# Performance work log

Measured on AMD Instinct MI355X. Metric: run time of the kernel, lower is better.

The kernel has to match this reference:

```python
import jax, jax.numpy as jnp
import numpy as np

N_EMBD = 2048
N_HEAD = 32
N_KV_HEAD = 8
HEAD_DIM = N_EMBD // N_HEAD  # 64
N_REP = N_HEAD // N_KV_HEAD  # 4
WINDOW = 1024
ROPE_BASE = 10000.0


def setup_inputs() -> dict:
    key = jax.random.key(0)
    ks = jax.random.split(key, 4)
    B, T = 2, 4096
    x = jax.random.normal(ks[0], (B, T, N_EMBD), dtype=jnp.float32)
    s = 0.02
    Wq = jax.random.normal(ks[1], (N_EMBD, N_HEAD * HEAD_DIM), dtype=jnp.float32) * s
    Wkv = jax.random.normal(ks[2], (N_EMBD, 2 * N_KV_HEAD * HEAD_DIM), dtype=jnp.float32) * s
    Wo = jax.random.normal(ks[3], (N_EMBD, N_EMBD), dtype=jnp.float32) * s
    return {"x": x, "Wq": Wq, "Wkv": Wkv, "Wo": Wo}


def _rotate_half(x):
    x1, x2 = jnp.split(x, 2, axis=-1)
    return jnp.concatenate([-x2, x1], axis=-1)


def _rope_cos_sin(T, dtype):
    inv_freq = 1.0 / (ROPE_BASE ** (jnp.arange(0, HEAD_DIM, 2, dtype=jnp.float32) / HEAD_DIM))
    t = jnp.arange(T, dtype=jnp.float32)
    freqs = jnp.einsum("i,j->ij", t, inv_freq)  # [T, HEAD_DIM/2]
    emb = jnp.concatenate([freqs, freqs], axis=-1)  # [T, HEAD_DIM]
    return jnp.cos(emb).astype(dtype)[None, None], jnp.sin(emb).astype(dtype)[None, None]


def reference(x, Wq, Wkv, Wo):
    B, T, _ = x.shape
    q = (x @ Wq).reshape(B, T, N_HEAD, HEAD_DIM).transpose(0, 2, 1, 3)  # [B,H,T,D]
    kv = (x @ Wkv).reshape(B, T, 2, N_KV_HEAD, HEAD_DIM)
    k = kv[:, :, 0].transpose(0, 2, 1, 3)  # [B,KV,T,D]
    v = kv[:, :, 1].transpose(0, 2, 1, 3)

    cos, sin = _rope_cos_sin(T, x.dtype)
    q = q * cos + _rotate_half(q) * sin
    k = k * cos + _rotate_half(k) * sin

    # repeat kv heads for GQA: [B,KV,T,D] -> [B,H,T,D]
    k = jnp.repeat(k, N_REP, axis=1)
    v = jnp.repeat(v, N_REP, axis=1)

    scale = 1.0 / jnp.sqrt(jnp.asarray(HEAD_DIM, dtype=x.dtype))
    scores = jnp.einsum("bhqd,bhkd->bhqk", q, k) * scale  # [B,H,T,T]

    # causal + sliding window mask: attend iff q - window < kpos <= qpos
    qpos = jnp.arange(T)[:, None]
    kpos = jnp.arange(T)[None, :]
    allowed = (kpos <= qpos) & (kpos > qpos - WINDOW)
    scores = jnp.where(allowed[None, None], scores, jnp.asarray(-jnp.inf, dtype=scores.dtype))

    attn = jax.nn.softmax(scores, axis=-1)
    out = jnp.einsum("bhqk,bhkd->bhqd", attn, v)  # [B,H,T,D]
    out = out.transpose(0, 2, 1, 3).reshape(B, T, N_EMBD)
    return out @ Wo
```

## Files before the change

### kernel.cpp

```cpp
#include <hip/hip_runtime.h>
#include <cstddef>

typedef unsigned short ushort_t;
typedef unsigned int uint32;

typedef __bf16   bf16x8 __attribute__((ext_vector_type(8)));
typedef __bf16   bf16x2 __attribute__((ext_vector_type(2)));
typedef __bf16   bf16x4 __attribute__((ext_vector_type(4)));
typedef float    f32x16 __attribute__((ext_vector_type(16)));
typedef float    f32x4  __attribute__((ext_vector_type(4)));
typedef ushort_t u16x8  __attribute__((ext_vector_type(8)));
typedef ushort_t u16x4  __attribute__((ext_vector_type(4)));
typedef uint32   u32x4  __attribute__((ext_vector_type(4)));
typedef uint32   u32x2  __attribute__((ext_vector_type(2)));

__device__ __forceinline__ ushort_t f2b(float f) {
  uint32 u = __builtin_bit_cast(uint32, f);
  u += 0x7fff + ((u >> 16) & 1);
  return (ushort_t)(u >> 16);
}

__device__ __forceinline__ f32x16 mfma32(bf16x8 a, bf16x8 b, f32x16 c) {
  return __builtin_amdgcn_mfma_f32_32x32x16_bf16(a, b, c, 0, 0, 0);
}

__device__ __forceinline__ void gload_lds16(const void* g, void* l) {
  __builtin_amdgcn_global_load_lds((const __attribute__((address_space(1))) void*)g,
                                   (__attribute__((address_space(3))) void*)l, 16, 0, 0);
}

__launch_bounds__(256)
__global__ void k_prep(const float* __restrict__ x, ushort_t* __restrict__ x_c, int nCvt,
                       const float* __restrict__ Wq, ushort_t* __restrict__ WqT,
                       const float* __restrict__ Wkv, ushort_t* __restrict__ WkvT,
                       const float* __restrict__ Wo, ushort_t* __restrict__ WoT,
                       float* __restrict__ cosT, float* __restrict__ sinT) {
  __shared__ __align__(16) ushort_t tile[64][72];
  const int tid = threadIdx.x;
  int bid = blockIdx.x;
  if (bid < 512) {
    int idx = bid * 256 + tid;
    int t = idx >> 5, j = idx & 31;
    float invf = __expf(-(float)j * (9.210340371976184f / 32.0f));
    float ang = (float)t * invf;
    cosT[idx] = cosf(ang);
    sinT[idx] = sinf(ang);
    return;
  }
  bid -= 512;
  if (bid < nCvt) {
    size_t i = ((size_t)bid * 256 + tid) * 8;
    f32x4 a = *(const f32x4*)(x + i);
    f32x4 b = *(const f32x4*)(x + i + 4);
    u16x8 v = {f2b(a[0]), f2b(a[1]), f2b(a[2]), f2b(a[3]),
               f2b(b[0]), f2b(b[1]), f2b(b[2]), f2b(b[3])};
    *(u16x8*)(x_c + i) = v;
    return;
  }
  bid -= nCvt;
  const float* W;
  ushort_t* Wt;
  int N;
  if (bid < 1024)      { W = Wq;  Wt = WqT;  N = 2048; }
  else if (bid < 1536) { W = Wkv; Wt = WkvT; N = 1024; bid -= 1024; }
  else                 { W = Wo;  Wt = WoT;  N = 2048; bid -= 1536; }
  const int K = 2048;
  int nbx = N >> 6;
  int bx = bid % nbx, by = bid / nbx;
  int r0 = by << 6, c0 = bx << 6;
#pragma unroll
  for (int p = 0; p < 2; p++) {
    int id = p * 256 + tid;
    int r = id >> 3, cs = id & 7;
    const float* src = W + (size_t)(r0 + r) * N + c0 + cs * 8;
    f32x4 a = *(const f32x4*)(src);
    f32x4 b = *(const f32x4*)(src + 4);
    u16x8 v = {f2b(a[0]), f2b(a[1]), f2b(a[2]), f2b(a[3]),
               f2b(b[0]), f2b(b[1]), f2b(b[2]), f2b(b[3])};
    *(u16x8*)&tile[r][cs * 8] = v;
  }
  __syncthreads();
#pragma unroll
  for (int p = 0; p < 2; p++) {
    int id = p * 256 + tid;
    int oc = id >> 3, ocs = id & 7;
    u16x8 v;
#pragma unroll
    for (int j = 0; j < 8; j++) v[j] = tile[ocs * 8 + j][oc];
    *(u16x8*)(Wt + (size_t)(c0 + oc) * K + r0 + ocs * 8) = v;
  }
}

__launch_bounds__(256)
__global__ void k_gemm_qkv(const ushort_t* __restrict__ A,
                           const ushort_t* __restrict__ BtQ,
                           const ushort_t* __restrict__ BtKV, int M,
                           ushort_t* __restrict__ qout, ushort_t* __restrict__ kout,
                           ushort_t* __restrict__ vout,
                           const float* __restrict__ cosT,
                           const float* __restrict__ sinT) {
  __shared__ __align__(16) ushort_t lds[2][2][128 * 32];
  const int tid = threadIdx.x;
  const int wave = tid >> 6, lane = tid & 63;
  const int l31 = lane & 31, hf = lane >> 5;
  const int K = 2048;
  const int bid = (int)blockIdx.x;
  const int blk = (bid & 7) * (int)(gridDim.x >> 3) + (bid >> 3);
  const int nQ = (M >> 7) << 4;
  const bool isQ = blk < nQ;
  int sub = isQ ? blk : blk - nQ;
  const int nTn = isQ ? 16 : 8;
  const ushort_t* Bt = isQ ? BtQ : BtKV;
  const int st = sub >> 4, si = sub & 15;
  const int nStc = nTn >> 2;
  const int stm = st / nStc, stn = st % nStc;
  const int bm = stm * 4 + (si >> 2), bn = stn * 4 + (si & 3);
  const int row0 = bm << 7, col0 = bn << 7;

  f32x16 acc[2][2] = {};

  auto stage = [&](int buf, int k0) {
#pragma unroll
    for (int side = 0; side < 2; side++) {
      const ushort_t* src = side ? Bt : A;
      int r0g = side ? col0 : row0;
#pragma unroll
      for (int i = 0; i < 2; i++) {
        int rl = wave * 32 + i * 16 + (lane >> 2);
        int cs = lane & 3;
        const ushort_t* gp = src + (size_t)(r0g + rl) * K + k0 + cs * 8;
        ushort_t* lp = &lds[buf][side][(wave * 32 + i * 16) * 32];
        gload_lds16(gp, lp);
      }
    }
  };

  stage(0, 0);
  __syncthreads();

  const int wm = wave >> 1, wn = wave & 1;
  const int nk = K >> 5;
  for (int kt = 0; kt < nk; kt++) {
    const int buf = kt & 1;
    if (kt + 1 < nk) stage(buf ^ 1, (kt + 1) << 5);
    const ushort_t* la = &lds[buf][0][0];
    const ushort_t* lb = &lds[buf][1][0];
#pragma unroll
    for (int ks = 0; ks < 2; ks++) {
      const int kc = ks * 2 + hf;
      bf16x8 af[2], bg[2];
#pragma unroll
      for (int mi = 0; mi < 2; mi++) {
        int r = wm * 64 + mi * 32 + l31;
        af[mi] = *(const bf16x8*)(la + r * 32 + kc * 8);
      }
#pragma unroll
      for (int ni = 0; ni < 2; ni++) {
        int r = wn * 64 + ni * 32 + l31;
        bg[ni] = *(const bf16x8*)(lb + r * 32 + kc * 8);
      }
#pragma unroll
      for (int mi = 0; mi < 2; mi++)
#pragma unroll
        for (int ni = 0; ni < 2; ni++)
          acc[mi][ni] = mfma32(af[mi], bg[ni], acc[mi][ni]);
    }
    __syncthreads();
  }

  if (isQ) {
    int cg = col0 + wn * 64 + l31;
#pragma unroll
    for (int mi = 0; mi < 2; mi++)
#pragma unroll
      for (int r = 0; r < 16; r++) {
        int rg = row0 + wm * 64 + mi * 32 + (r & 3) + 8 * (r >> 2) + 4 * hf;
        int t = rg & 4095;
        float c = cosT[t * 32 + l31];
        float s = sinT[t * 32 + l31];
        float lo = acc[mi][0][r], hi = acc[mi][1][r];
        qout[(size_t)rg * 2048 + cg]      = f2b(lo * c - hi * s);
        qout[(size_t)rg * 2048 + cg + 32] = f2b(hi * c + lo * s);
      }
  } else {
    int cb = col0 + wn * 64;
    if (cb < 512) {
      int g = cb >> 6;
#pragma unroll
      for (int mi = 0; mi < 2; mi++)
#pragma unroll
        for (int r = 0; r < 16; r++) {
          int rg = row0 + wm * 64 + mi * 32 + (r & 3) + 8 * (r >> 2) + 4 * hf;
          int t = rg & 4095, b = rg >> 12;
          float c = cosT[t * 32 + l31];
          float s = sinT[t * 32 + l31];
          float lo = acc[mi][0][r], hi = acc[mi][1][r];
          size_t base = ((size_t)(b * 8 + g) * 4096 + t) * 64;
          kout[base + l31]      = f2b(lo * c - hi * s);
          kout[base + l31 + 32] = f2b(hi * c + lo * s);
        }
    } else {
#pragma unroll
      for (int mi = 0; mi < 2; mi++)
#pragma unroll
        for (int ni = 0; ni < 2; ni++) {
          int vd = cb + ni * 32 + l31 - 512;
          int g = vd >> 6, d = vd & 63;
#pragma unroll
          for (int g2 = 0; g2 < 4; g2++) {
            int rg = row0 + wm * 64 + mi * 32 + 8 * g2 + 4 * hf;
            int b = rg >> 12, tl = rg & 4095;
            u16x4 pk = {f2b(acc[mi][ni][g2 * 4 + 0]), f2b(acc[mi][ni][g2 * 4 + 1]),
                        f2b(acc[mi][ni][g2 * 4 + 2]), f2b(acc[mi][ni][g2 * 4 + 3])};
            size_t base = (((size_t)(b * 8 + g) * 128 + (tl >> 5)) * 64 + d) * 32;
            int vtl = 16 * (g2 >> 1) + 8 * hf + 4 * (g2 & 1);
            *(u16x4*)(vout + base + vtl) = pk;
          }
        }
    }
  }
}

__launch_bounds__(256)
__global__ void k_gemm_o(const ushort_t* __restrict__ A, const ushort_t* __restrict__ Bt,
                         int M, float* __restrict__ outf) {
  __shared__ __align__(16) ushort_t lds[2][2][128 * 32];
  const int tid = threadIdx.x;
  const int wave = tid >> 6, lane = tid & 63;
  const int l31 = lane & 31, hf = lane >> 5;
  const int K = 2048, N = 2048, nTn = 16;
  const int bid = (int)blockIdx.x;
  const int blk = (bid & 7) * (int)(gridDim.x >> 3) + (bid >> 3);
  const int st = blk >> 4, si = blk & 15;
  const int nStc = nTn >> 2;
  const int stm = st / nStc, stn = st % nStc;
  const int bm = stm * 4 + (si >> 2), bn = stn * 4 + (si & 3);
  const int row0 = bm << 7, col0 = bn << 7;

  f32x16 acc[2][2] = {};

  auto stage = [&](int buf, int k0) {
#pragma unroll
    for (int side = 0; side < 2; side++) {
      const ushort_t* src = side ? Bt : A;
      int r0g = side ? col0 : row0;
#pragma unroll
      for (int i = 0; i < 2; i++) {
        int rl = wave * 32 + i * 16 + (lane >> 2);
        int cs = lane & 3;
        const ushort_t* gp = src + (size_t)(r0g + rl) * K + k0 + cs * 8;
        ushort_t* lp = &lds[buf][side][(wave * 32 + i * 16) * 32];
        gload_lds16(gp, lp);
      }
    }
  };

  stage(0, 0);
  __syncthreads();

  const int wm = wave >> 1, wn = wave & 1;
  const int nk = K >> 5;
  for (int kt = 0; kt < nk; kt++) {
    const int buf = kt & 1;
    if (kt + 1 < nk) stage(buf ^ 1, (kt + 1) << 5);
    const ushort_t* la = &lds[buf][0][0];
    const ushort_t* lb = &lds[buf][1][0];
#pragma unroll
    for (int ks = 0; ks < 2; ks++) {
      const int kc = ks * 2 + hf;
      bf16x8 af[2], bg[2];
#pragma unroll
      for (int mi = 0; mi < 2; mi++) {
        int r = wm * 64 + mi * 32 + l31;
        af[mi] = *(const bf16x8*)(la + r * 32 + kc * 8);
      }
#pragma unroll
      for (int ni = 0; ni < 2; ni++) {
        int r = wn * 64 + ni * 32 + l31;
        bg[ni] = *(const bf16x8*)(lb + r * 32 + kc * 8);
      }
#pragma unroll
      for (int mi = 0; mi < 2; mi++)
#pragma unroll
        for (int ni = 0; ni < 2; ni++)
          acc[mi][ni] = mfma32(af[mi], bg[ni], acc[mi][ni]);
    }
    __syncthreads();
  }

#pragma unroll
  for (int mi = 0; mi < 2; mi++)
#pragma unroll
    for (int ni = 0; ni < 2; ni++) {
      int cg = col0 + wn * 64 + ni * 32 + l31;
#pragma unroll
      for (int r = 0; r < 16; r++) {
        int rg = row0 + wm * 64 + mi * 32 + (r & 3) + 8 * (r >> 2) + 4 * hf;
        outf[(size_t)rg * N + cg] = acc[mi][ni][r];
      }
    }
}

__launch_bounds__(256)
__global__ void k_attn(ushort_t* __restrict__ q, const ushort_t* __restrict__ kk,
                       const ushort_t* __restrict__ vT) {
  __shared__ __align__(16) ushort_t Kl[2][32][68];
  __shared__ __align__(16) ushort_t Vl[2][64][36];
  const int tid = threadIdx.x;
  const int wave = tid >> 6, lane = tid & 63;
  const int l31 = lane & 31, hf = lane >> 5;
  const int chunk = gridDim.x >> 3;
  const int blk = ((int)blockIdx.x & 7) * chunk + ((int)blockIdx.x >> 3);
  const int bh = blk >> 5, qt4 = 31 - (blk & 31);
  const int b = bh >> 5, hd = bh & 31;
  const int g = hd >> 2;
  const int qt = qt4 * 4 + wave;
  const int t0 = qt << 5;
  const float NEG = -1e30f;
  const float C = 0.18033688011112042f;
  const float M0 = 10.0f;

  const ushort_t* qp = q + ((size_t)(b * 4096 + t0 + l31)) * 2048 + hd * 64 + hf * 8;
  bf16x8 qf[4];
#pragma unroll
  for (int ks = 0; ks < 4; ks++) qf[ks] = *(const bf16x8*)(qp + ks * 16);

  const ushort_t* kg = kk + (size_t)(b * 8 + g) * 4096 * 64;
  const ushort_t* vg = vT + (size_t)(b * 8 + g) * 128 * 64 * 32;

  f32x16 o[2] = {};
  float l_i = 0.f;

  const int KT0 = (qt4 >= 8) ? ((qt4 * 128 - 1023) >> 5) : 0;
  const int KTmax = qt4 * 4 + 3;

  const int krow = tid >> 3, kchk = tid & 7;
  const int vrow = tid >> 2, vchk = tid & 3;

  {
    u32x4 kv = *(const u32x4*)(kg + ((size_t)(KT0 << 5) + krow) * 64 + kchk * 8);
    u32x4 vv = *(const u32x4*)(vg + (size_t)KT0 * 2048 + vrow * 32 + vchk * 8);
    *(u32x2*)&Kl[0][krow][kchk * 8]     = (u32x2){kv[0], kv[1]};
    *(u32x2*)&Kl[0][krow][kchk * 8 + 4] = (u32x2){kv[2], kv[3]};
    *(u32x2*)&Vl[0][vrow][vchk * 8]     = (u32x2){vv[0], vv[1]};
    *(u32x2*)&Vl[0][vrow][vchk * 8 + 4] = (u32x2){vv[2], vv[3]};
  }
  __syncthreads();

  for (int kt = KT0; kt <= KTmax; kt++) {
    const int buf = (kt - KT0) & 1;
    const int kb = kt << 5;
    const bool more = (kt < KTmax);

    u32x4 kv, vv;
    if (more) {
      kv = *(const u32x4*)(kg + ((size_t)(kb + 32) + krow) * 64 + kchk * 8);
      vv = *(const u32x4*)(vg + (size_t)(kt + 1) * 2048 + vrow * 32 + vchk * 8);
    }

    const bool live = (kt <= qt) && (kb > t0 - 1055);
    if (live) {
      bf16x8 kf[4];
#pragma unroll
      for (int ks = 0; ks < 4; ks++) {
        u32x2 a0 = *(const u32x2*)&Kl[buf][l31][hf * 8 + ks * 16];
        u32x2 a1 = *(const u32x2*)&Kl[buf][l31][hf * 8 + ks * 16 + 4];
        u32x4 w = {a0[0], a0[1], a1[0], a1[1]};
        kf[ks] = __builtin_bit_cast(bf16x8, w);
      }
      f32x16 sa = {};
      __builtin_amdgcn_s_setprio(1);
#pragma unroll
      for (int ks = 0; ks < 4; ks++) sa = mfma32(kf[ks], qf[ks], sa);
      __builtin_amdgcn_s_setprio(0);

      bf16x8 vf[2][2];
#pragma unroll
      for (int ks = 0; ks < 2; ks++)
#pragma unroll
        for (int mi = 0; mi < 2; mi++) {
          u32x2 a0 = *(const u32x2*)&Vl[buf][mi * 32 + l31][hf * 8 + ks * 16];
          u32x2 a1 = *(const u32x2*)&Vl[buf][mi * 32 + l31][hf * 8 + ks * 16 + 4];
          u32x4 w = {a0[0], a0[1], a1[0], a1[1]};
          vf[ks][mi] = __builtin_bit_cast(bf16x8, w);
        }

      const bool need_mask = (kt == qt) || (kb < t0 - 992);
      if (need_mask) {
        int base = (t0 + l31) - kb - 4 * hf;
#pragma unroll
        for (int r = 0; r < 16; r++) {
          int off = (r & 3) + 8 * (r >> 2);
          sa[r] = ((unsigned)(base - off) < 1024u) ? sa[r] : NEG;
        }
      }
      float p[16];
#pragma unroll
      for (int r = 0; r < 16; r++)
        p[r] = __builtin_amdgcn_exp2f(__builtin_fmaf(sa[r], C, -M0));
      l_i += (((p[0] + p[1]) + (p[2] + p[3])) + ((p[4] + p[5]) + (p[6] + p[7]))) +
             (((p[8] + p[9]) + (p[10] + p[11])) + ((p[12] + p[13]) + (p[14] + p[15])));

      uint32 u[8];
#pragma unroll
      for (int i = 0; i < 8; i++) {
        bf16x2 t2 = {(__bf16)p[2 * i], (__bf16)p[2 * i + 1]};
        u[i] = __builtin_bit_cast(uint32, t2);
      }

#pragma unroll
      for (int ks = 0; ks < 2; ks++) {
        u32x4 fr = {u[4 * ks + 0], u[4 * ks + 1], u[4 * ks + 2], u[4 * ks + 3]};
        bf16x8 pf = __builtin_bit_cast(bf16x8, fr);
        __builtin_amdgcn_s_setprio(1);
        o[0] = mfma32(vf[ks][0], pf, o[0]);
        o[1] = mfma32(vf[ks][1], pf, o[1]);
        __builtin_amdgcn_s_setprio(0);
      }
    }

    if (more) {
      *(u32x2*)&Kl[buf ^ 1][krow][kchk * 8]     = (u32x2){kv[0], kv[1]};
      *(u32x2*)&Kl[buf ^ 1][krow][kchk * 8 + 4] = (u32x2){kv[2], kv[3]};
      *(u32x2*)&Vl[buf ^ 1][vrow][vchk * 8]     = (u32x2){vv[0], vv[1]};
      *(u32x2*)&Vl[buf ^ 1][vrow][vchk * 8 + 4] = (u32x2){vv[2], vv[3]};
    }
    __syncthreads();
  }

  l_i += __shfl_xor(l_i, 32, 64);
  float inv_l = 1.0f / fmaxf(l_i, 1e-30f);
  ushort_t* op = q + ((size_t)(b * 4096 + t0 + l31)) * 2048 + hd * 64;
#pragma unroll
  for (int mi = 0; mi < 2; mi++)
#pragma unroll
    for (int g2 = 0; g2 < 4; g2++) {
      int d0 = mi * 32 + 8 * g2 + 4 * hf;
      bf16x4 pk = {(__bf16)(o[mi][g2 * 4 + 0] * inv_l), (__bf16)(o[mi][g2 * 4 + 1] * inv_l),
                   (__bf16)(o[mi][g2 * 4 + 2] * inv_l), (__bf16)(o[mi][g2 * 4 + 3] * inv_l)};
      *(bf16x4*)(op + d0) = pk;
    }
}

extern "C" void kernel_launch(void* const* d_in, const int* in_sizes, int n_in,
                              void* d_out, int out_size, void* d_ws, size_t ws_size,
                              hipStream_t stream) {
  const float* x   = (const float*)d_in[0];
  const float* Wq  = (const float*)d_in[1];
  const float* Wkv = (const float*)d_in[2];
  const float* Wo  = (const float*)d_in[3];
  float* outp = (float*)d_out;

  const int BT = in_sizes[0] / 2048;
  const int Bb = BT / 4096;

  char* ob = (char*)d_out;
  const size_t MB = 1024 * 1024;
  ushort_t* x_c  = (ushort_t*)(ob);
  ushort_t* WqT  = (ushort_t*)(ob + 32 * MB);
  ushort_t* WkvT = (ushort_t*)(ob + 40 * MB);
  ushort_t* kbuf = (ushort_t*)(ob + 44 * MB);
  ushort_t* vbuf = (ushort_t*)(ob + 52 * MB);
  float*    cosT = (float*)   (ob + 60 * MB);
  float*    sinT = (float*)   (ob + 60 * MB + 512 * 1024);

  char* ws = (char*)d_ws;
  ushort_t* qbuf = (ushort_t*)(ws);
  ushort_t* WoT  = (ushort_t*)(ws + 32 * MB);

  const int nCvt = BT;
  k_prep<<<512 + nCvt + 2560, 256, 0, stream>>>(x, x_c, nCvt, Wq, WqT, Wkv, WkvT,
                                                Wo, WoT, cosT, sinT);

  k_gemm_qkv<<<(BT / 128) * 24, 256, 0, stream>>>(
      x_c, WqT, WkvT, BT, qbuf, kbuf, vbuf, cosT, sinT);

  k_attn<<<Bb * 32 * 32, 256, 0, stream>>>(qbuf, kbuf, vbuf);

  k_gemm_o<<<(BT / 128) * 16, 256, 0, stream>>>(qbuf, WoT, BT, outp);
}
```

Baseline: 459.4 us.

## Process two K/V tiles per barrier and fold softmax scale into Q

The attention loop now stages two 32-key K/V tiles per shared-memory buffer and processes both between barriers. This halves the number of __syncthreads and loop-control steps, and issues two tiles of global prefetch at once, at the cost of doubling LDS usage. The softmax scale (log2e/sqrt(d)) is now applied in the Q projection epilogue, and the fixed -10 exponent offset is dropped, which removes one FMA per score. Without that offset, exp2 has less headroom against overflow on large scores.

```diff
diff --git a/kernel.cpp b/kernel.cpp
--- a/kernel.cpp
+++ b/kernel.cpp
@@ -169,6 +169,7 @@
   }
 
   if (isQ) {
+    const float SC = 0.18033688011112042f;
     int cg = col0 + wn * 64 + l31;
 #pragma unroll
     for (int mi = 0; mi < 2; mi++)
@@ -179,8 +180,8 @@
         float c = cosT[t * 32 + l31];
         float s = sinT[t * 32 + l31];
         float lo = acc[mi][0][r], hi = acc[mi][1][r];
-        qout[(size_t)rg * 2048 + cg]      = f2b(lo * c - hi * s);
-        qout[(size_t)rg * 2048 + cg + 32] = f2b(hi * c + lo * s);
+        qout[(size_t)rg * 2048 + cg]      = f2b((lo * c - hi * s) * SC);
+        qout[(size_t)rg * 2048 + cg + 32] = f2b((hi * c + lo * s) * SC);
       }
   } else {
     int cb = col0 + wn * 64;
@@ -304,8 +305,8 @@
 __launch_bounds__(256)
 __global__ void k_attn(ushort_t* __restrict__ q, const ushort_t* __restrict__ kk,
                        const ushort_t* __restrict__ vT) {
-  __shared__ __align__(16) ushort_t Kl[2][32][68];
-  __shared__ __align__(16) ushort_t Vl[2][64][36];
+  __shared__ __align__(16) ushort_t Kl[2][64][68];
+  __shared__ __align__(16) ushort_t Vl[2][128][36];
   const int tid = threadIdx.x;
   const int wave = tid >> 6, lane = tid & 63;
   const int l31 = lane & 31, hf = lane >> 5;
@@ -317,8 +318,6 @@
   const int qt = qt4 * 4 + wave;
   const int t0 = qt << 5;
   const float NEG = -1e30f;
-  const float C = 0.18033688011112042f;
-  const float M0 = 10.0f;
 
   const ushort_t* qp = q + ((size_t)(b * 4096 + t0 + l31)) * 2048 + hd * 64 + hf * 8;
   bf16x8 qf[4];
@@ -332,98 +331,110 @@
   float l_i = 0.f;
 
   const int KT0 = (qt4 >= 8) ? ((qt4 * 128 - 1023) >> 5) : 0;
+  const int KT0e = KT0 & ~1;
   const int KTmax = qt4 * 4 + 3;
 
   const int krow = tid >> 3, kchk = tid & 7;
   const int vrow = tid >> 2, vchk = tid & 3;
 
-  {
-    u32x4 kv = *(const u32x4*)(kg + ((size_t)(KT0 << 5) + krow) * 64 + kchk * 8);
-    u32x4 vv = *(const u32x4*)(vg + (size_t)KT0 * 2048 + vrow * 32 + vchk * 8);
-    *(u32x2*)&Kl[0][krow][kchk * 8]     = (u32x2){kv[0], kv[1]};
-    *(u32x2*)&Kl[0][krow][kchk * 8 + 4] = (u32x2){kv[2], kv[3]};
-    *(u32x2*)&Vl[0][vrow][vchk * 8]     = (u32x2){vv[0], vv[1]};
-    *(u32x2*)&Vl[0][vrow][vchk * 8 + 4] = (u32x2){vv[2], vv[3]};
+#pragma unroll
+  for (int j = 0; j < 2; j++) {
+    u32x4 kv = *(const u32x4*)(kg + ((size_t)((KT0e + j) << 5) + krow) * 64 + kchk * 8);
+    u32x4 vv = *(const u32x4*)(vg + (size_t)(KT0e + j) * 2048 + vrow * 32 + vchk * 8);
+    *(u32x2*)&Kl[0][j * 32 + krow][kchk * 8]     = (u32x2){kv[0], kv[1]};
+    *(u32x2*)&Kl[0][j * 32 + krow][kchk * 8 + 4] = (u32x2){kv[2], kv[3]};
+    *(u32x2*)&Vl[0][j * 64 + vrow][vchk * 8]     = (u32x2){vv[0], vv[1]};
+    *(u32x2*)&Vl[0][j * 64 + vrow][vchk * 8 + 4] = (u32x2){vv[2], vv[3]};
   }
   __syncthreads();
 
-  for (int kt = KT0; kt <= KTmax; kt++) {
-    const int buf = (kt - KT0) & 1;
-    const int kb = kt << 5;
-    const bool more = (kt < KTmax);
-
-    u32x4 kv, vv;
+  for (int kt = KT0e; kt <= KTmax; kt += 2) {
+    const int buf = ((kt - KT0e) >> 1) & 1;
+    const bool more = (kt + 2 <= KTmax);
+
+    u32x4 kv[2], vv[2];
     if (more) {
-      kv = *(const u32x4*)(kg + ((size_t)(kb + 32) + krow) * 64 + kchk * 8);
-      vv = *(const u32x4*)(vg + (size_t)(kt + 1) * 2048 + vrow * 32 + vchk * 8);
-    }
-
-    const bool live = (kt <= qt) && (kb > t0 - 1055);
-    if (live) {
-      bf16x8 kf[4];
-#pragma unroll
-      for (int ks = 0; ks < 4; ks++) {
-        u32x2 a0 = *(const u32x2*)&Kl[buf][l31][hf * 8 + ks * 16];
-        u32x2 a1 = *(const u32x2*)&Kl[buf][l31][hf * 8 + ks * 16 + 4];
-        u32x4 w = {a0[0], a0[1], a1[0], a1[1]};
-        kf[ks] = __builtin_bit_cast(bf16x8, w);
-      }
-      f32x16 sa = {};
-      __builtin_amdgcn_s_setprio(1);
-#pragma unroll
-      for (int ks = 0; ks < 4; ks++) sa = mfma32(kf[ks], qf[ks], sa);
-      __builtin_amdgcn_s_setprio(0);
-
-      bf16x8 vf[2][2];
-#pragma unroll
-      for (int ks = 0; ks < 2; ks++)
-#pragma unroll
-        for (int mi = 0; mi < 2; mi++) {
-          u32x2 a0 = *(const u32x2*)&Vl[buf][mi * 32 + l31][hf * 8 + ks * 16];
-          u32x2 a1 = *(const u32x2*)&Vl[buf][mi * 32 + l31][hf * 8 + ks * 16 + 4];
+#pragma unroll
+      for (int j = 0; j < 2; j++) {
+        kv[j] = *(const u32x4*)(kg + ((size_t)((kt + 2 + j) << 5) + krow) * 64 + kchk * 8);
+        vv[j] = *(const u32x4*)(vg + (size_t)(kt + 2 + j) * 2048 + vrow * 32 + vchk * 8);
+      }
+    }
+
+#pragma unroll
+    for (int j = 0; j < 2; j++) {
+      const int ktj = kt + j;
+      const int kb = ktj << 5;
+      const bool live = (ktj <= qt) && (kb > t0 - 1055);
+      if (live) {
+        bf16x8 kf[4];
+#pragma unroll
+        for (int ks = 0; ks < 4; ks++) {
+          u32x2 a0 = *(const u32x2*)&Kl[buf][j * 32 + l31][hf * 8 + ks * 16];
+          u32x2 a1 = *(const u32x2*)&Kl[buf][j * 32 + l31][hf * 8 + ks * 16 + 4];
           u32x4 w = {a0[0], a0[1], a1[0], a1[1]};
-          vf[ks][mi] = __builtin_bit_cast(bf16x8, w);
-        }
-
-      const bool need_mask = (kt == qt) || (kb < t0 - 992);
-      if (need_mask) {
-        int base = (t0 + l31) - kb - 4 * hf;
-#pragma unroll
-        for (int r = 0; r < 16; r++) {
-          int off = (r & 3) + 8 * (r >> 2);
-          sa[r] = ((unsigned)(base - off) < 1024u) ? sa[r] : NEG;
-        }
-      }
-      float p[16];
-#pragma unroll
-      for (int r = 0; r < 16; r++)
-        p[r] = __builtin_amdgcn_exp2f(__builtin_fmaf(sa[r], C, -M0));
-      l_i += (((p[0] + p[1]) + (p[2] + p[3])) + ((p[4] + p[5]) + (p[6] + p[7]))) +
-             (((p[8] + p[9]) + (p[10] + p[11])) + ((p[12] + p[13]) + (p[14] + p[15])));
-
-      uint32 u[8];
-#pragma unroll
-      for (int i = 0; i < 8; i++) {
-        bf16x2 t2 = {(__bf16)p[2 * i], (__bf16)p[2 * i + 1]};
-        u[i] = __builtin_bit_cast(uint32, t2);
-      }
-
-#pragma unroll
-      for (int ks = 0; ks < 2; ks++) {
-        u32x4 fr = {u[4 * ks + 0], u[4 * ks + 1], u[4 * ks + 2], u[4 * ks + 3]};
-        bf16x8 pf = __builtin_bit_cast(bf16x8, fr);
+          kf[ks] = __builtin_bit_cast(bf16x8, w);
+        }
+        f32x16 sa = {};
         __builtin_amdgcn_s_setprio(1);
-        o[0] = mfma32(vf[ks][0], pf, o[0]);
-        o[1] = mfma32(vf[ks][1], pf, o[1]);
+#pragma unroll
+        for (int ks = 0; ks < 4; ks++) sa = mfma32(kf[ks], qf[ks], sa);
         __builtin_amdgcn_s_setprio(0);
+
+        bf16x8 vf[2][2];
+#pragma unroll
+        for (int ks = 0; ks < 2; ks++)
+#pragma unroll
+          for (int mi = 0; mi < 2; mi++) {
+            u32x2 a0 = *(const u32x2*)&Vl[buf][j * 64 + mi * 32 + l31][hf * 8 + ks * 16];
+            u32x2 a1 = *(const u32x2*)&Vl[buf][j * 64 + mi * 32 + l31][hf * 8 + ks * 16 + 4];
+            u32x4 w = {a0[0], a0[1], a1[0], a1[1]};
+            vf[ks][mi] = __builtin_bit_cast(bf16x8, w);
+          }
+
+        const bool need_mask = (ktj == qt) || (kb < t0 - 992);
+        if (need_mask) {
+          int base = (t0 + l31) - kb - 4 * hf;
+#pragma unroll
+          for (int r = 0; r < 16; r++) {
+            int off = (r & 3) + 8 * (r >> 2);
+            sa[r] = ((unsigned)(base - off) < 1024u) ? sa[r] : NEG;
+          }
+        }
+        float p[16];
+#pragma unroll
+        for (int r = 0; r < 16; r++)
+          p[r] = __builtin_amdgcn_exp2f(sa[r]);
+        l_i += (((p[0] + p[1]) + (p[2] + p[3])) + ((p[4] + p[5]) + (p[6] + p[7]))) +
+               (((p[8] + p[9]) + (p[10] + p[11])) + ((p[12] + p[13]) + (p[14] + p[15])));
+
+        uint32 u[8];
+#pragma unroll
+        for (int i = 0; i < 8; i++) {
+          bf16x2 t2 = {(__bf16)p[2 * i], (__bf16)p[2 * i + 1]};
+          u[i] = __builtin_bit_cast(uint32, t2);
+        }
+
+#pragma unroll
+        for (int ks = 0; ks < 2; ks++) {
+          u32x4 fr = {u[4 * ks + 0], u[4 * ks + 1], u[4 * ks + 2], u[4 * ks + 3]};
+          bf16x8 pf = __builtin_bit_cast(bf16x8, fr);
+          __builtin_amdgcn_s_setprio(1);
+          o[0] = mfma32(vf[ks][0], pf, o[0]);
+          o[1] = mfma32(vf[ks][1], pf, o[1]);
+          __builtin_amdgcn_s_setprio(0);
+        }
       }
     }
 
     if (more) {
-      *(u32x2*)&Kl[buf ^ 1][krow][kchk * 8]     = (u32x2){kv[0], kv[1]};
-      *(u32x2*)&Kl[buf ^ 1][krow][kchk * 8 + 4] = (u32x2){kv[2], kv[3]};
-      *(u32x2*)&Vl[buf ^ 1][vrow][vchk * 8]     = (u32x2){vv[0], vv[1]};
-      *(u32x2*)&Vl[buf ^ 1][vrow][vchk * 8 + 4] = (u32x2){vv[2], vv[3]};
+#pragma unroll
+      for (int j = 0; j < 2; j++) {
+        *(u32x2*)&Kl[buf ^ 1][j * 32 + krow][kchk * 8]     = (u32x2){kv[j][0], kv[j][1]};
+        *(u32x2*)&Kl[buf ^ 1][j * 32 + krow][kchk * 8 + 4] = (u32x2){kv[j][2], kv[j][3]};
+        *(u32x2*)&Vl[buf ^ 1][j * 64 + vrow][vchk * 8]     = (u32x2){vv[j][0], vv[j][1]};
+        *(u32x2*)&Vl[buf ^ 1][j * 64 + vrow][vchk * 8 + 4] = (u32x2){vv[j][2], vv[j][3]};
+      }
     }
     __syncthreads();
   }
```

Measured after the change: 455.0 us (median of 2 runs). No clear change (-1.0%).
